# Kernel optimization log

Hardware: AMD Instinct MI355X
Metric: run time of the kernel (lower is better)

Reference implementation:

```python
import jax, jax.numpy as jnp
import numpy as np

SOFT_TAU = 0.5
MAX_TEMP = 40.0
LABEL_SMOOTH = 0.1


def setup_inputs() -> dict:
    key = jax.random.key(0)
    k1, k2 = jax.random.split(key)
    B, Tv, Tw, D = 64, 128, 128, 256
    video_features = jax.random.normal(k1, (B, Tv, D), dtype=jnp.float32)
    wifi_features = jax.random.normal(k2, (B, Tw, D), dtype=jnp.float32)
    logit_scale = jnp.ones((), dtype=jnp.float32)
    return {"video_features": video_features, "wifi_features": wifi_features, "logit_scale": logit_scale}


def _cross_entropy_ls(logits, labels):
    # torch CrossEntropyLoss(label_smoothing=0.1), mean reduction
    logp = jax.nn.log_softmax(logits, axis=-1)
    nll = -jnp.take_along_axis(logp, labels[:, None], axis=1)[:, 0]
    smooth = -jnp.mean(logp, axis=-1)
    return jnp.mean((1.0 - LABEL_SMOOTH) * nll + LABEL_SMOOTH * smooth)


def reference(video_features, wifi_features, logit_scale):
    B = video_features.shape[0]
    # [B, B, Tv, Tw] dense cross-modal similarity
    sim = jnp.einsum('imd,jnd->ijmn', video_features, wifi_features)
    sim_d = jax.lax.stop_gradient(sim)
    # video->wifi soft pooling over Tw
    attn_v2w = jax.nn.softmax(sim_d / SOFT_TAU, axis=3)
    soft_sim_v2w = jnp.sum(sim * attn_v2w, axis=3)  # [B, B, Tv]
    # wifi->video soft pooling over Tv
    attn_w2v = jax.nn.softmax(sim_d / SOFT_TAU, axis=2)
    soft_sim_w2v = jnp.sum(sim * attn_w2v, axis=2)  # [B, B, Tw]
    # frame-level softmax pooling to global similarity
    fw_v = jax.nn.softmax(jax.lax.stop_gradient(soft_sim_v2w) / SOFT_TAU, axis=2)
    sim_v2w_global = jnp.sum(soft_sim_v2w * fw_v, axis=2)  # [B, B]
    fw_w = jax.nn.softmax(jax.lax.stop_gradient(soft_sim_w2v) / SOFT_TAU, axis=2)
    sim_w2v_global = jnp.sum(soft_sim_w2v * fw_w, axis=2)  # [B, B]
    dense_similarity = (sim_v2w_global + sim_w2v_global) / 2.0
    scale = jnp.minimum(logit_scale, MAX_TEMP)
    logits_per_video = scale * dense_similarity
    logits_per_wifi = logits_per_video.T
    labels = jnp.arange(B, dtype=jnp.int32)
    loss_video = _cross_entropy_ls(logits_per_video, labels)
    loss_wifi = _cross_entropy_ls(logits_per_wifi, labels)
    return (loss_video + loss_wifi) / 2.0
```

## Files before the change

kernel.cpp:

```cpp
#include <hip/hip_runtime.h>
#include <hip/hip_bf16.h>

typedef __attribute__((ext_vector_type(8))) short bf16x8;
typedef __attribute__((ext_vector_type(16))) float f32x16;
typedef __attribute__((ext_vector_type(4))) unsigned short u16x4;

#define TT 128
#define DD 256
#define BK 64

__device__ __forceinline__ unsigned short f2bf(float f) {
  unsigned int x = __float_as_uint(f);
  x += 0x7fffu + ((x >> 16) & 1u);
  return (unsigned short)(x >> 16);
}

__device__ __forceinline__ bf16x8 pack8(float4 lo, float4 hi) {
  bf16x8 v;
  v[0] = (short)f2bf(lo.x); v[1] = (short)f2bf(lo.y);
  v[2] = (short)f2bf(lo.z); v[3] = (short)f2bf(lo.w);
  v[4] = (short)f2bf(hi.x); v[5] = (short)f2bf(hi.y);
  v[6] = (short)f2bf(hi.z); v[7] = (short)f2bf(hi.w);
  return v;
}

__global__ __launch_bounds__(256) void conv_kernel(
    const float* __restrict__ v, const float* __restrict__ w,
    unsigned short* __restrict__ vb, unsigned short* __restrict__ wb) {
  const int idx = blockIdx.x * 256 + threadIdx.x;
  float4 a = reinterpret_cast<const float4*>(v)[idx];
  float4 b = reinterpret_cast<const float4*>(w)[idx];
  u16x4 pa, pb;
  pa[0] = f2bf(a.x); pa[1] = f2bf(a.y); pa[2] = f2bf(a.z); pa[3] = f2bf(a.w);
  pb[0] = f2bf(b.x); pb[1] = f2bf(b.y); pb[2] = f2bf(b.z); pb[3] = f2bf(b.w);
  reinterpret_cast<u16x4*>(vb)[idx] = pa;
  reinterpret_cast<u16x4*>(wb)[idx] = pb;
}

template <bool PRE>
__global__ __launch_bounds__(512, 4) void pair_kernel(
    const float* __restrict__ videof, const float* __restrict__ wifif,
    const unsigned short* __restrict__ videob,
    const unsigned short* __restrict__ wifib,
    float* __restrict__ dense) {
  __shared__ __align__(16) char lds[73728];
  const int tid = threadIdx.x;
  const int bid = blockIdx.x;
  const int bi = bid >> 6, bj = bid & 63;
  const int wid = tid >> 6, l = tid & 63;
  const int l31 = l & 31;

  const int o  = wid >> 2;
  const int mg = wid & 1;
  const int cg = (wid >> 1) & 1;

  const char* vsrc = (const char*)videob + (size_t)bi * (TT * DD * 2);
  const char* wsrc = (const char*)wifib  + (size_t)bj * (TT * DD * 2);
  const int grow8 = l >> 3;
  const int gcb   = ((l & 7) ^ grow8) << 4;
  const int srow = tid >> 2;
  const int scb  = (tid & 3) * 32;
  const int sswz = (srow & 7) << 4;
  const int sb0  = srow * 128 + ((scb) ^ sswz);
  const int sb1  = srow * 128 + ((scb + 16) ^ sswz);

  f32x16 acc[2][2];
#pragma unroll
  for (int mi = 0; mi < 2; ++mi)
#pragma unroll
    for (int t = 0; t < 2; ++t)
#pragma unroll
      for (int r = 0; r < 16; ++r) acc[mi][t][r] = 0.f;

  const int apan = o ? 16384 : 0;
  const int bpan = o ? 0 : 16384;
  const int xr   = (l & 7) << 4;
  const int khalf = (l >> 5) * 16;
  const int x0 = (mg * 64 + l31) * 128;
  const int x1 = (mg * 64 + 32 + l31) * 128;
  const int y0 = (cg * 64 + l31) * 128;
  const int y1 = (cg * 64 + 32 + l31) * 128;

#define STAGE_PRE(KP, BUF)                                                    \
  do {                                                                        \
    _Pragma("unroll") for (int k_ = 0; k_ < 4; ++k_) {                        \
      const int q_ = wid * 4 + k_;                                            \
      const int c_ = q_ & 15;                                                 \
      const char* s_ = ((q_ < 16) ? vsrc : wsrc) + (c_ * 8 + grow8) * 512 +   \
                       (KP) * 128 + gcb;                                      \
      char* d_ = lds + (BUF) * 32768 + ((q_ < 16) ? 0 : 16384) + c_ * 1024;   \
      __builtin_amdgcn_global_load_lds((const void*)s_, (void*)d_, 16, 0, 0); \
    }                                                                         \
  } while (0)

#define STAGE_REG(KP, BUF)                                                    \
  do {                                                                        \
    const float* pa_ = videof + (size_t)bi * (TT * DD) + srow * DD +          \
                       (KP) * BK + (tid & 3) * 16;                            \
    const float* pb_ = wifif + (size_t)bj * (TT * DD) + srow * DD +           \
                       (KP) * BK + (tid & 3) * 16;                            \
    float4 a0_ = *(const float4*)(pa_);                                       \
    float4 a1_ = *(const float4*)(pa_ + 4);                                   \
    float4 a2_ = *(const float4*)(pa_ + 8);                                   \
    float4 a3_ = *(const float4*)(pa_ + 12);                                  \
    float4 b0_ = *(const float4*)(pb_);                                       \
    float4 b1_ = *(const float4*)(pb_ + 4);                                   \
    float4 b2_ = *(const float4*)(pb_ + 8);                                   \
    float4 b3_ = *(const float4*)(pb_ + 12);                                  \
    char* base_ = lds + (BUF) * 32768;                                        \
    *(bf16x8*)(base_ + sb0)         = pack8(a0_, a1_);                        \
    *(bf16x8*)(base_ + sb1)         = pack8(a2_, a3_);                        \
    *(bf16x8*)(base_ + 16384 + sb0) = pack8(b0_, b1_);                        \
    *(bf16x8*)(base_ + 16384 + sb1) = pack8(b2_, b3_);                        \
  } while (0)

  if constexpr (PRE) STAGE_PRE(0, 0); else STAGE_REG(0, 0);
  __syncthreads();

  for (int kp = 0; kp < 4; ++kp) {
    const int bufoff = (kp & 1) * 32768;
    if (kp < 3) {
      if constexpr (PRE) STAGE_PRE(kp + 1, (kp + 1) & 1);
      else STAGE_REG(kp + 1, (kp + 1) & 1);
    }
#pragma unroll
    for (int ks = 0; ks < 4; ++ks) {
      const int cb = ks * 32 + khalf;
      bf16x8 ax0 = *(const bf16x8*)(lds + bufoff + apan + x0 + (cb ^ xr));
      bf16x8 ax1 = *(const bf16x8*)(lds + bufoff + apan + x1 + (cb ^ xr));
      bf16x8 by0 = *(const bf16x8*)(lds + bufoff + bpan + y0 + (cb ^ xr));
      bf16x8 by1 = *(const bf16x8*)(lds + bufoff + bpan + y1 + (cb ^ xr));
      acc[0][0] = __builtin_amdgcn_mfma_f32_32x32x16_bf16(ax0, by0, acc[0][0], 0, 0, 0);
      acc[0][1] = __builtin_amdgcn_mfma_f32_32x32x16_bf16(ax0, by1, acc[0][1], 0, 0, 0);
      acc[1][0] = __builtin_amdgcn_mfma_f32_32x32x16_bf16(ax1, by0, acc[1][0], 0, 0, 0);
      acc[1][1] = __builtin_amdgcn_mfma_f32_32x32x16_bf16(ax1, by1, acc[1][1], 0, 0, 0);
    }
    __syncthreads();
  }

  float* PM = (float*)(lds + 65536);
  float* PS = PM + 512;
  float* PV = PM + 1024;
  float* Gb = PM + 1536;
  const int colb = cg * 64;

#pragma unroll
  for (int t = 0; t < 2; ++t) {
    float mx = acc[0][t][0];
#pragma unroll
    for (int mi = 0; mi < 2; ++mi)
#pragma unroll
      for (int r = 0; r < 16; ++r) mx = fmaxf(mx, acc[mi][t][r]);
    mx = fmaxf(mx, __shfl_xor(mx, 32));
    if (l < 32) PM[o * 256 + mg * 128 + colb + t * 32 + l] = mx;
  }
  __syncthreads();

#pragma unroll
  for (int t = 0; t < 2; ++t) {
    const int c = colb + t * 32 + l31;
    const float mx = fmaxf(PM[o * 256 + c], PM[o * 256 + 128 + c]);
    float se = 0.f, sv = 0.f;
#pragma unroll
    for (int mi = 0; mi < 2; ++mi)
#pragma unroll
      for (int r = 0; r < 16; ++r) {
        const float v = acc[mi][t][r];
        const float e = __expf((v - mx) * 2.0f);
        se += e;
        sv = fmaf(e, v, sv);
      }
    se += __shfl_xor(se, 32);
    sv += __shfl_xor(sv, 32);
    if (l < 32) {
      PS[o * 256 + mg * 128 + c] = se;
      PV[o * 256 + mg * 128 + c] = sv;
    }
  }
  __syncthreads();

  if (wid < 2) {
    const int oo = wid == 0 ? 1 : 0;
    const float* PSo = PS + oo * 256;
    const float* PVo = PV + oo * 256;
    float a0 = (PVo[l] + PVo[128 + l]) / (PSo[l] + PSo[128 + l]);
    float a1 = (PVo[64 + l] + PVo[192 + l]) / (PSo[64 + l] + PSo[192 + l]);
    float mx = fmaxf(a0, a1);
#pragma unroll
    for (int s = 1; s < 64; s <<= 1) mx = fmaxf(mx, __shfl_xor(mx, s));
    float e0 = __expf((a0 - mx) * 2.0f), e1 = __expf((a1 - mx) * 2.0f);
    float se = e0 + e1, sev = e0 * a0 + e1 * a1;
#pragma unroll
    for (int s = 1; s < 64; s <<= 1) { se += __shfl_xor(se, s); sev += __shfl_xor(sev, s); }
    if (l == 0) Gb[wid] = sev / se;
  }
  __syncthreads();
  if (tid == 0) dense[bid] = 0.5f * (Gb[0] + Gb[1]);
}

__global__ __launch_bounds__(64) void loss_kernel(
    const float* __restrict__ dense, const float* __restrict__ scalep,
    float* __restrict__ out) {
  const int i = threadIdx.x;
  const float sc = fminf(scalep[0], 40.0f);
  float mxr = -3.4e38f, mxc = -3.4e38f;
  for (int j = 0; j < 64; ++j) {
    mxr = fmaxf(mxr, sc * dense[i * 64 + j]);
    mxc = fmaxf(mxc, sc * dense[j * 64 + i]);
  }
  float ser = 0.f, sec = 0.f, slr = 0.f, slc = 0.f;
  for (int j = 0; j < 64; ++j) {
    float zr = sc * dense[i * 64 + j];
    float zc = sc * dense[j * 64 + i];
    ser += __expf(zr - mxr); sec += __expf(zc - mxc);
    slr += zr;               slc += zc;
  }
  const float lser = mxr + logf(ser);
  const float lsec = mxc + logf(sec);
  const float zd = sc * dense[i * 65];
  float lv = lser - 0.9f * zd - 0.1f * (slr * (1.0f / 64.0f));
  float lw = lsec - 0.9f * zd - 0.1f * (slc * (1.0f / 64.0f));
  float t = 0.5f * (lv + lw);
#pragma unroll
  for (int s = 1; s < 64; s <<= 1) t += __shfl_xor(t, s);
  if (i == 0) out[0] = t * (1.0f / 64.0f);
}

extern "C" void kernel_launch(void* const* d_in, const int* in_sizes, int n_in,
                              void* d_out, int out_size, void* d_ws, size_t ws_size,
                              hipStream_t stream) {
  (void)in_sizes; (void)n_in; (void)out_size;
  const float* video = (const float*)d_in[0];
  const float* wifi  = (const float*)d_in[1];
  const float* scale = (const float*)d_in[2];
  float* dense = (float*)d_ws;
  unsigned short* vb = (unsigned short*)((char*)d_ws + 16384);
  unsigned short* wb = vb + 64 * TT * DD;

  const bool pre = ws_size >= (size_t)16384 + 2u * 64 * TT * DD * 2;
  if (pre) {
    hipLaunchKernelGGL(conv_kernel, dim3(2048), dim3(256), 0, stream,
                       video, wifi, vb, wb);
    hipLaunchKernelGGL((pair_kernel<true>), dim3(64 * 64), dim3(512), 0, stream,
                       video, wifi, vb, wb, dense);
  } else {
    hipLaunchKernelGGL((pair_kernel<false>), dim3(64 * 64), dim3(512), 0, stream,
                       video, wifi, vb, wb, dense);
  }
  hipLaunchKernelGGL(loss_kernel, dim3(1), dim3(64), 0, stream,
                     dense, scale, (float*)d_out);
}
```

Before: 101.7 us.

## Halve pair-kernel block to 4 waves, each computing a 64x128 MFMA tile

Shrinks the pair kernel from 8 to 4 wavefronts per block. Each wave now holds a 2x4 grid of 32x32 MFMA accumulators covering all 128 columns instead of 2x2, and staging loops issue twice as many loads per thread. This raises register-level reuse of A fragments and cuts cross-wave LDS traffic. The cost is doubled accumulator registers, which lowers occupancy (launch bounds 256,2), and less parallelism for hiding load latency.

```diff
diff --git a/kernel.cpp b/kernel.cpp
--- a/kernel.cpp
+++ b/kernel.cpp
@@ -38,7 +38,7 @@
 }
 
 template <bool PRE>
-__global__ __launch_bounds__(512, 4) void pair_kernel(
+__global__ __launch_bounds__(256, 2) void pair_kernel(
     const float* __restrict__ videof, const float* __restrict__ wifif,
     const unsigned short* __restrict__ videob,
     const unsigned short* __restrict__ wifib,
@@ -50,41 +50,36 @@
   const int wid = tid >> 6, l = tid & 63;
   const int l31 = l & 31;
 
-  const int o  = wid >> 2;
+  const int o  = wid >> 1;
   const int mg = wid & 1;
-  const int cg = (wid >> 1) & 1;
 
   const char* vsrc = (const char*)videob + (size_t)bi * (TT * DD * 2);
   const char* wsrc = (const char*)wifib  + (size_t)bj * (TT * DD * 2);
   const int grow8 = l >> 3;
   const int gcb   = ((l & 7) ^ grow8) << 4;
-  const int srow = tid >> 2;
-  const int scb  = (tid & 3) * 32;
+  const int srow = tid >> 1;
+  const int scb  = (tid & 1) * 64;
   const int sswz = (srow & 7) << 4;
-  const int sb0  = srow * 128 + ((scb) ^ sswz);
-  const int sb1  = srow * 128 + ((scb + 16) ^ sswz);
-
-  f32x16 acc[2][2];
+
+  f32x16 acc[2][4];
 #pragma unroll
   for (int mi = 0; mi < 2; ++mi)
 #pragma unroll
-    for (int t = 0; t < 2; ++t)
+    for (int t = 0; t < 4; ++t)
 #pragma unroll
       for (int r = 0; r < 16; ++r) acc[mi][t][r] = 0.f;
 
   const int apan = o ? 16384 : 0;
   const int bpan = o ? 0 : 16384;
-  const int xr   = (l & 7) << 4;
+  const int xr    = (l & 7) << 4;
   const int khalf = (l >> 5) * 16;
   const int x0 = (mg * 64 + l31) * 128;
-  const int x1 = (mg * 64 + 32 + l31) * 128;
-  const int y0 = (cg * 64 + l31) * 128;
-  const int y1 = (cg * 64 + 32 + l31) * 128;
+  const int y0 = l31 * 128;
 
 #define STAGE_PRE(KP, BUF)                                                    \
   do {                                                                        \
-    _Pragma("unroll") for (int k_ = 0; k_ < 4; ++k_) {                        \
-      const int q_ = wid * 4 + k_;                                            \
+    _Pragma("unroll") for (int k_ = 0; k_ < 8; ++k_) {                        \
+      const int q_ = wid * 8 + k_;                                            \
       const int c_ = q_ & 15;                                                 \
       const char* s_ = ((q_ < 16) ? vsrc : wsrc) + (c_ * 8 + grow8) * 512 +   \
                        (KP) * 128 + gcb;                                      \
@@ -96,22 +91,26 @@
 #define STAGE_REG(KP, BUF)                                                    \
   do {                                                                        \
     const float* pa_ = videof + (size_t)bi * (TT * DD) + srow * DD +          \
-                       (KP) * BK + (tid & 3) * 16;                            \
+                       (KP) * BK + (tid & 1) * 32;                            \
     const float* pb_ = wifif + (size_t)bj * (TT * DD) + srow * DD +           \
-                       (KP) * BK + (tid & 3) * 16;                            \
-    float4 a0_ = *(const float4*)(pa_);                                       \
-    float4 a1_ = *(const float4*)(pa_ + 4);                                   \
-    float4 a2_ = *(const float4*)(pa_ + 8);                                   \
-    float4 a3_ = *(const float4*)(pa_ + 12);                                  \
-    float4 b0_ = *(const float4*)(pb_);                                       \
-    float4 b1_ = *(const float4*)(pb_ + 4);                                   \
-    float4 b2_ = *(const float4*)(pb_ + 8);                                   \
-    float4 b3_ = *(const float4*)(pb_ + 12);                                  \
+                       (KP) * BK + (tid & 1) * 32;                            \
     char* base_ = lds + (BUF) * 32768;                                        \
-    *(bf16x8*)(base_ + sb0)         = pack8(a0_, a1_);                        \
-    *(bf16x8*)(base_ + sb1)         = pack8(a2_, a3_);                        \
-    *(bf16x8*)(base_ + 16384 + sb0) = pack8(b0_, b1_);                        \
-    *(bf16x8*)(base_ + 16384 + sb1) = pack8(b2_, b3_);                        \
+    _Pragma("unroll") for (int h_ = 0; h_ < 2; ++h_) {                        \
+      float4 a0_ = *(const float4*)(pa_ + h_ * 16);                           \
+      float4 a1_ = *(const float4*)(pa_ + h_ * 16 + 4);                       \
+      float4 a2_ = *(const float4*)(pa_ + h_ * 16 + 8);                       \
+      float4 a3_ = *(const float4*)(pa_ + h_ * 16 + 12);                      \
+      float4 b0_ = *(const float4*)(pb_ + h_ * 16);                           \
+      float4 b1_ = *(const float4*)(pb_ + h_ * 16 + 4);                       \
+      float4 b2_ = *(const float4*)(pb_ + h_ * 16 + 8);                       \
+      float4 b3_ = *(const float4*)(pb_ + h_ * 16 + 12);                      \
+      const int c0_ = srow * 128 + ((scb + h_ * 32) ^ sswz);                  \
+      const int c1_ = srow * 128 + ((scb + h_ * 32 + 16) ^ sswz);             \
+      *(bf16x8*)(base_ + c0_)         = pack8(a0_, a1_);                      \
+      *(bf16x8*)(base_ + c1_)         = pack8(a2_, a3_);                      \
+      *(bf16x8*)(base_ + 16384 + c0_) = pack8(b0_, b1_);                      \
+      *(bf16x8*)(base_ + 16384 + c1_) = pack8(b2_, b3_);                      \
+    }                                                                         \
   } while (0)
 
   if constexpr (PRE) STAGE_PRE(0, 0); else STAGE_REG(0, 0);
@@ -126,14 +125,22 @@
 #pragma unroll
     for (int ks = 0; ks < 4; ++ks) {
       const int cb = ks * 32 + khalf;
-      bf16x8 ax0 = *(const bf16x8*)(lds + bufoff + apan + x0 + (cb ^ xr));
-      bf16x8 ax1 = *(const bf16x8*)(lds + bufoff + apan + x1 + (cb ^ xr));
-      bf16x8 by0 = *(const bf16x8*)(lds + bufoff + bpan + y0 + (cb ^ xr));
-      bf16x8 by1 = *(const bf16x8*)(lds + bufoff + bpan + y1 + (cb ^ xr));
+      const char* xb = lds + bufoff + apan;
+      const char* yb = lds + bufoff + bpan;
+      bf16x8 ax0 = *(const bf16x8*)(xb + x0 + (cb ^ xr));
+      bf16x8 ax1 = *(const bf16x8*)(xb + x0 + 4096 + (cb ^ xr));
+      bf16x8 by0 = *(const bf16x8*)(yb + y0 + (cb ^ xr));
+      bf16x8 by1 = *(const bf16x8*)(yb + y0 + 4096 + (cb ^ xr));
+      bf16x8 by2 = *(const bf16x8*)(yb + y0 + 8192 + (cb ^ xr));
+      bf16x8 by3 = *(const bf16x8*)(yb + y0 + 12288 + (cb ^ xr));
       acc[0][0] = __builtin_amdgcn_mfma_f32_32x32x16_bf16(ax0, by0, acc[0][0], 0, 0, 0);
       acc[0][1] = __builtin_amdgcn_mfma_f32_32x32x16_bf16(ax0, by1, acc[0][1], 0, 0, 0);
+      acc[0][2] = __builtin_amdgcn_mfma_f32_32x32x16_bf16(ax0, by2, acc[0][2], 0, 0, 0);
+      acc[0][3] = __builtin_amdgcn_mfma_f32_32x32x16_bf16(ax0, by3, acc[0][3], 0, 0, 0);
       acc[1][0] = __builtin_amdgcn_mfma_f32_32x32x16_bf16(ax1, by0, acc[1][0], 0, 0, 0);
       acc[1][1] = __builtin_amdgcn_mfma_f32_32x32x16_bf16(ax1, by1, acc[1][1], 0, 0, 0);
+      acc[1][2] = __builtin_amdgcn_mfma_f32_32x32x16_bf16(ax1, by2, acc[1][2], 0, 0, 0);
+      acc[1][3] = __builtin_amdgcn_mfma_f32_32x32x16_bf16(ax1, by3, acc[1][3], 0, 0, 0);
     }
     __syncthreads();
   }
@@ -142,23 +149,22 @@
   float* PS = PM + 512;
   float* PV = PM + 1024;
   float* Gb = PM + 1536;
-  const int colb = cg * 64;
-
-#pragma unroll
-  for (int t = 0; t < 2; ++t) {
+
+#pragma unroll
+  for (int t = 0; t < 4; ++t) {
     float mx = acc[0][t][0];
 #pragma unroll
     for (int mi = 0; mi < 2; ++mi)
 #pragma unroll
       for (int r = 0; r < 16; ++r) mx = fmaxf(mx, acc[mi][t][r]);
     mx = fmaxf(mx, __shfl_xor(mx, 32));
-    if (l < 32) PM[o * 256 + mg * 128 + colb + t * 32 + l] = mx;
-  }
-  __syncthreads();
-
-#pragma unroll
-  for (int t = 0; t < 2; ++t) {
-    const int c = colb + t * 32 + l31;
+    if (l < 32) PM[o * 256 + mg * 128 + t * 32 + l] = mx;
+  }
+  __syncthreads();
+
+#pragma unroll
+  for (int t = 0; t < 4; ++t) {
+    const int c = t * 32 + l31;
     const float mx = fmaxf(PM[o * 256 + c], PM[o * 256 + 128 + c]);
     float se = 0.f, sv = 0.f;
 #pragma unroll
@@ -241,10 +247,10 @@
   if (pre) {
     hipLaunchKernelGGL(conv_kernel, dim3(2048), dim3(256), 0, stream,
                        video, wifi, vb, wb);
-    hipLaunchKernelGGL((pair_kernel<true>), dim3(64 * 64), dim3(512), 0, stream,
+    hipLaunchKernelGGL((pair_kernel<true>), dim3(64 * 64), dim3(256), 0, stream,
                        video, wifi, vb, wb, dense);
   } else {
-    hipLaunchKernelGGL((pair_kernel<false>), dim3(64 * 64), dim3(512), 0, stream,
+    hipLaunchKernelGGL((pair_kernel<false>), dim3(64 * 64), dim3(256), 0, stream,
                        video, wifi, vb, wb, dense);
   }
   hipLaunchKernelGGL(loss_kernel, dim3(1), dim3(64), 0, stream,
```

Result: faster. 97.41 us (-4.2%).

## Pad LDS row groups and use online-softmax partial merge in epilogue

Applied to the files above, without the earlier changes.

Changes the shared-memory tile layout so each 8-row group is padded to a 1056-byte stride, which is meant to reduce bank conflicts on MFMA operand reads. It also replaces the two-pass max/exp softmax epilogue with a per-half online softmax: each half keeps its own max, and the halves are merged with rescaling, which removes one block-wide barrier round. Exponentials move to exp2f with a folded log2e·2 constant. LDS usage grows slightly and an extra merge stage is added.

```diff
diff --git a/kernel.cpp b/kernel.cpp
--- a/kernel.cpp
+++ b/kernel.cpp
@@ -8,6 +8,11 @@
 #define TT 128
 #define DD 256
 #define BK 64
+#define CP 1056
+#define PAN (16 * CP)
+#define BUFSZ (2 * PAN)
+#define PART (2 * BUFSZ)
+#define K2L 2.8853900817779268f
 
 __device__ __forceinline__ unsigned short f2bf(float f) {
   unsigned int x = __float_as_uint(f);
@@ -43,7 +48,7 @@
     const unsigned short* __restrict__ videob,
     const unsigned short* __restrict__ wifib,
     float* __restrict__ dense) {
-  __shared__ __align__(16) char lds[73728];
+  __shared__ __align__(16) char lds[73744];
   const int tid = threadIdx.x;
   const int bid = blockIdx.x;
   const int bi = bid >> 6, bj = bid & 63;
@@ -61,8 +66,7 @@
   const int srow = tid >> 2;
   const int scb  = (tid & 3) * 32;
   const int sswz = (srow & 7) << 4;
-  const int sb0  = srow * 128 + ((scb) ^ sswz);
-  const int sb1  = srow * 128 + ((scb + 16) ^ sswz);
+  const int srbase = (srow >> 3) * CP + (srow & 7) * 128;
 
   f32x16 acc[2][2];
 #pragma unroll
@@ -72,14 +76,14 @@
 #pragma unroll
       for (int r = 0; r < 16; ++r) acc[mi][t][r] = 0.f;
 
-  const int apan = o ? 16384 : 0;
-  const int bpan = o ? 0 : 16384;
-  const int xr   = (l & 7) << 4;
+  const int apan = o ? PAN : 0;
+  const int bpan = o ? 0 : PAN;
+  const int xr    = (l31 & 7) << 4;
   const int khalf = (l >> 5) * 16;
-  const int x0 = (mg * 64 + l31) * 128;
-  const int x1 = (mg * 64 + 32 + l31) * 128;
-  const int y0 = (cg * 64 + l31) * 128;
-  const int y1 = (cg * 64 + 32 + l31) * 128;
+  const int xrow  = mg * 64 + l31;
+  const int ycol  = cg * 64 + l31;
+  const int xbase = (xrow >> 3) * CP + (xrow & 7) * 128;
+  const int ybase = (ycol >> 3) * CP + (ycol & 7) * 128;
 
 #define STAGE_PRE(KP, BUF)                                                    \
   do {                                                                        \
@@ -88,7 +92,7 @@
       const int c_ = q_ & 15;                                                 \
       const char* s_ = ((q_ < 16) ? vsrc : wsrc) + (c_ * 8 + grow8) * 512 +   \
                        (KP) * 128 + gcb;                                      \
-      char* d_ = lds + (BUF) * 32768 + ((q_ < 16) ? 0 : 16384) + c_ * 1024;   \
+      char* d_ = lds + (BUF) * BUFSZ + ((q_ < 16) ? 0 : PAN) + c_ * CP;       \
       __builtin_amdgcn_global_load_lds((const void*)s_, (void*)d_, 16, 0, 0); \
     }                                                                         \
   } while (0)
@@ -107,29 +111,33 @@
     float4 b1_ = *(const float4*)(pb_ + 4);                                   \
     float4 b2_ = *(const float4*)(pb_ + 8);                                   \
     float4 b3_ = *(const float4*)(pb_ + 12);                                  \
-    char* base_ = lds + (BUF) * 32768;                                        \
-    *(bf16x8*)(base_ + sb0)         = pack8(a0_, a1_);                        \
-    *(bf16x8*)(base_ + sb1)         = pack8(a2_, a3_);                        \
-    *(bf16x8*)(base_ + 16384 + sb0) = pack8(b0_, b1_);                        \
-    *(bf16x8*)(base_ + 16384 + sb1) = pack8(b2_, b3_);                        \
+    char* base_ = lds + (BUF) * BUFSZ;                                        \
+    const int c0_ = srbase + ((scb) ^ sswz);                                  \
+    const int c1_ = srbase + ((scb + 16) ^ sswz);                             \
+    *(bf16x8*)(base_ + c0_)       = pack8(a0_, a1_);                          \
+    *(bf16x8*)(base_ + c1_)       = pack8(a2_, a3_);                          \
+    *(bf16x8*)(base_ + PAN + c0_) = pack8(b0_, b1_);                          \
+    *(bf16x8*)(base_ + PAN + c1_) = pack8(b2_, b3_);                          \
   } while (0)
 
   if constexpr (PRE) STAGE_PRE(0, 0); else STAGE_REG(0, 0);
   __syncthreads();
 
   for (int kp = 0; kp < 4; ++kp) {
-    const int bufoff = (kp & 1) * 32768;
+    const int bufoff = (kp & 1) * BUFSZ;
     if (kp < 3) {
       if constexpr (PRE) STAGE_PRE(kp + 1, (kp + 1) & 1);
       else STAGE_REG(kp + 1, (kp + 1) & 1);
     }
+    const char* xb = lds + bufoff + apan + xbase;
+    const char* yb = lds + bufoff + bpan + ybase;
 #pragma unroll
     for (int ks = 0; ks < 4; ++ks) {
-      const int cb = ks * 32 + khalf;
-      bf16x8 ax0 = *(const bf16x8*)(lds + bufoff + apan + x0 + (cb ^ xr));
-      bf16x8 ax1 = *(const bf16x8*)(lds + bufoff + apan + x1 + (cb ^ xr));
-      bf16x8 by0 = *(const bf16x8*)(lds + bufoff + bpan + y0 + (cb ^ xr));
-      bf16x8 by1 = *(const bf16x8*)(lds + bufoff + bpan + y1 + (cb ^ xr));
+      const int off = (ks * 32 + khalf) ^ xr;
+      bf16x8 ax0 = *(const bf16x8*)(xb + off);
+      bf16x8 ax1 = *(const bf16x8*)(xb + 4 * CP + off);
+      bf16x8 by0 = *(const bf16x8*)(yb + off);
+      bf16x8 by1 = *(const bf16x8*)(yb + 4 * CP + off);
       acc[0][0] = __builtin_amdgcn_mfma_f32_32x32x16_bf16(ax0, by0, acc[0][0], 0, 0, 0);
       acc[0][1] = __builtin_amdgcn_mfma_f32_32x32x16_bf16(ax0, by1, acc[0][1], 0, 0, 0);
       acc[1][0] = __builtin_amdgcn_mfma_f32_32x32x16_bf16(ax1, by0, acc[1][0], 0, 0, 0);
@@ -138,58 +146,65 @@
     __syncthreads();
   }
 
-  float* PM = (float*)(lds + 65536);
+  float* PM = (float*)(lds + PART);
   float* PS = PM + 512;
   float* PV = PM + 1024;
   float* Gb = PM + 1536;
-  const int colb = cg * 64;
 
 #pragma unroll
   for (int t = 0; t < 2; ++t) {
     float mx = acc[0][t][0];
 #pragma unroll
-    for (int mi = 0; mi < 2; ++mi)
-#pragma unroll
-      for (int r = 0; r < 16; ++r) mx = fmaxf(mx, acc[mi][t][r]);
-    mx = fmaxf(mx, __shfl_xor(mx, 32));
-    if (l < 32) PM[o * 256 + mg * 128 + colb + t * 32 + l] = mx;
-  }
-  __syncthreads();
-
-#pragma unroll
-  for (int t = 0; t < 2; ++t) {
-    const int c = colb + t * 32 + l31;
-    const float mx = fmaxf(PM[o * 256 + c], PM[o * 256 + 128 + c]);
+    for (int r = 1; r < 16; ++r) mx = fmaxf(mx, acc[0][t][r]);
+#pragma unroll
+    for (int r = 0; r < 16; ++r) mx = fmaxf(mx, acc[1][t][r]);
+    const float mxk = mx * K2L;
     float se = 0.f, sv = 0.f;
 #pragma unroll
     for (int mi = 0; mi < 2; ++mi)
 #pragma unroll
       for (int r = 0; r < 16; ++r) {
         const float v = acc[mi][t][r];
-        const float e = __expf((v - mx) * 2.0f);
+        const float e = exp2f(fmaf(v, K2L, -mxk));
         se += e;
         sv = fmaf(e, v, sv);
       }
-    se += __shfl_xor(se, 32);
-    sv += __shfl_xor(sv, 32);
+    const float om = __shfl_xor(mx, 32);
+    const float os = __shfl_xor(se, 32);
+    const float ov = __shfl_xor(sv, 32);
+    const float M  = fmaxf(mx, om);
+    const float f1 = exp2f((mx - M) * K2L);
+    const float f2 = exp2f((om - M) * K2L);
+    se = fmaf(se, f1, os * f2);
+    sv = fmaf(sv, f1, ov * f2);
     if (l < 32) {
-      PS[o * 256 + mg * 128 + c] = se;
-      PV[o * 256 + mg * 128 + c] = sv;
+      const int idx = o * 256 + mg * 128 + cg * 64 + t * 32 + l;
+      PM[idx] = M; PS[idx] = se; PV[idx] = sv;
     }
   }
   __syncthreads();
 
+  if (tid < 256) {
+    const int o2 = tid >> 7, c = tid & 127;
+    const int i0 = o2 * 256 + c, i1 = i0 + 128;
+    const float m0 = PM[i0], m1 = PM[i1];
+    const float M  = fmaxf(m0, m1);
+    const float f0 = exp2f((m0 - M) * K2L);
+    const float f1 = exp2f((m1 - M) * K2L);
+    const float s  = fmaf(PS[i0], f0, PS[i1] * f1);
+    const float v  = fmaf(PV[i0], f0, PV[i1] * f1);
+    PM[i0] = v / s;
+  }
+  __syncthreads();
+
   if (wid < 2) {
-    const int oo = wid == 0 ? 1 : 0;
-    const float* PSo = PS + oo * 256;
-    const float* PVo = PV + oo * 256;
-    float a0 = (PVo[l] + PVo[128 + l]) / (PSo[l] + PSo[128 + l]);
-    float a1 = (PVo[64 + l] + PVo[192 + l]) / (PSo[64 + l] + PSo[192 + l]);
+    const float* RS = PM + (wid == 0 ? 256 : 0);
+    float a0 = RS[l], a1 = RS[64 + l];
     float mx = fmaxf(a0, a1);
 #pragma unroll
     for (int s = 1; s < 64; s <<= 1) mx = fmaxf(mx, __shfl_xor(mx, s));
-    float e0 = __expf((a0 - mx) * 2.0f), e1 = __expf((a1 - mx) * 2.0f);
-    float se = e0 + e1, sev = e0 * a0 + e1 * a1;
+    float e0 = exp2f((a0 - mx) * K2L), e1 = exp2f((a1 - mx) * K2L);
+    float se = e0 + e1, sev = fmaf(e0, a0, e1 * a1);
 #pragma unroll
     for (int s = 1; s < 64; s <<= 1) { se += __shfl_xor(se, s); sev += __shfl_xor(sev, s); }
     if (l == 0) Gb[wid] = sev / se;
```

Result: slower. 111.2 us (+9.4%).

## Keep video fragments in registers and loop over sixteen wifi clips per block

Applied to the files above, without the earlier changes.

The pair kernel becomes persistent-style: 256 blocks, each loading one video clip's bf16 fragments into registers once and streaming 16 wifi clips through double-buffered LDS halves. The per-pair epilogue now does an online max/sum merge with exp2 instead of an extra LDS max pass and barrier. The final reduction overlaps the next clip's loads and writes results via atomicAdd into zero-initialised outputs. This trades grid parallelism (256 blocks, launch bound lowered to 2 waves/EU) and heavier register use for less redundant video loading and fewer barriers.

```diff
diff --git a/kernel.cpp b/kernel.cpp
--- a/kernel.cpp
+++ b/kernel.cpp
@@ -7,7 +7,9 @@
 
 #define TT 128
 #define DD 256
-#define BK 64
+#define HBUF 32768
+#define PARTOFF 65536
+#define K2L 2.8853900817779268f
 
 __device__ __forceinline__ unsigned short f2bf(float f) {
   unsigned int x = __float_as_uint(f);
@@ -37,165 +39,196 @@
   reinterpret_cast<u16x4*>(wb)[idx] = pb;
 }
 
+#define FR(BUF, ROW, KSLOT)                                                   \
+  (*(const bf16x8*)(lds + (BUF) * HBUF + (ROW) * 256 +                        \
+                    ((((KSLOT)) ^ ((ROW) & 15)) << 4)))
+
 template <bool PRE>
-__global__ __launch_bounds__(512, 4) void pair_kernel(
+__global__ __launch_bounds__(512, 2) void pair_kernel(
     const float* __restrict__ videof, const float* __restrict__ wifif,
     const unsigned short* __restrict__ videob,
     const unsigned short* __restrict__ wifib,
     float* __restrict__ dense) {
-  __shared__ __align__(16) char lds[73728];
+  __shared__ __align__(16) char lds[77824];
   const int tid = threadIdx.x;
   const int bid = blockIdx.x;
-  const int bi = bid >> 6, bj = bid & 63;
+  const int i  = bid >> 2, jg = bid & 3;
   const int wid = tid >> 6, l = tid & 63;
   const int l31 = l & 31;
+  const int khalf = l >> 5;
 
   const int o  = wid >> 2;
   const int mg = wid & 1;
   const int cg = (wid >> 1) & 1;
 
-  const char* vsrc = (const char*)videob + (size_t)bi * (TT * DD * 2);
-  const char* wsrc = (const char*)wifib  + (size_t)bj * (TT * DD * 2);
-  const int grow8 = l >> 3;
-  const int gcb   = ((l & 7) ^ grow8) << 4;
-  const int srow = tid >> 2;
-  const int scb  = (tid & 3) * 32;
-  const int sswz = (srow & 7) << 4;
-  const int sb0  = srow * 128 + ((scb) ^ sswz);
-  const int sb1  = srow * 128 + ((scb + 16) ^ sswz);
+  if (tid < 16) dense[i * 64 + jg * 16 + tid] = 0.0f;
+
+  const char* vsrc  = (const char*)videob + (size_t)i * (TT * DD * 2);
+  const char* wsrc0 = (const char*)wifib + (size_t)(jg * 16) * (TT * DD * 2);
+  const float* vsrcf  = videof + (size_t)i * (TT * DD);
+  const float* wsrcf0 = wifif + (size_t)(jg * 16) * (TT * DD);
+
+  const int crow  = l >> 4;
+  const int cslot = l & 15;
+  const int frow = tid >> 2, fq = tid & 3;
+
+  const int vbase = (o ? cg : mg) * 64;
+  const int wbase = (o ? mg : cg) * 64;
+
+#define STAGE_PRE_(SRC, KH, BUF)                                              \
+  do {                                                                        \
+    _Pragma("unroll") for (int k_ = 0; k_ < 4; ++k_) {                        \
+      const int c_ = wid * 4 + k_;                                            \
+      const int r_ = c_ * 4 + crow;                                           \
+      const char* s_ = (SRC) + r_ * 512 + (KH) * 256 +                        \
+                       ((cslot ^ (r_ & 15)) << 4);                            \
+      char* d_ = lds + (BUF) * HBUF + c_ * 1024;                              \
+      __builtin_amdgcn_global_load_lds((const void*)s_, (void*)d_, 16, 0, 0); \
+    }                                                                         \
+  } while (0)
+
+#define STAGE_REG_(SRCF, KH, BUF)                                             \
+  do {                                                                        \
+    _Pragma("unroll") for (int s_ = 0; s_ < 4; ++s_) {                        \
+      const int slot_ = fq * 4 + s_;                                          \
+      const float* p_ = (SRCF) + frow * DD + (KH) * 128 + slot_ * 8;          \
+      float4 x0_ = *(const float4*)(p_);                                      \
+      float4 x1_ = *(const float4*)(p_ + 4);                                  \
+      *(bf16x8*)(lds + (BUF) * HBUF + frow * 256 +                            \
+                 ((slot_ ^ (frow & 15)) << 4)) = pack8(x0_, x1_);             \
+    }                                                                         \
+  } while (0)
+
+  if constexpr (PRE) STAGE_PRE_(vsrc, 0, 0); else STAGE_REG_(vsrcf, 0, 0);
+  __syncthreads();
+  if constexpr (PRE) STAGE_PRE_(vsrc, 1, 1); else STAGE_REG_(vsrcf, 1, 1);
+  bf16x8 vf[2][16];
+#pragma unroll
+  for (int g = 0; g < 2; ++g)
+#pragma unroll
+    for (int ksl = 0; ksl < 8; ++ksl)
+      vf[g][ksl] = FR(0, vbase + g * 32 + l31, 2 * ksl + khalf);
+  __syncthreads();
+  if constexpr (PRE) STAGE_PRE_(wsrc0, 0, 0); else STAGE_REG_(wsrcf0, 0, 0);
+#pragma unroll
+  for (int g = 0; g < 2; ++g)
+#pragma unroll
+    for (int ksl = 0; ksl < 8; ++ksl)
+      vf[g][8 + ksl] = FR(1, vbase + g * 32 + l31, 2 * ksl + khalf);
+  __syncthreads();
 
   f32x16 acc[2][2];
-#pragma unroll
-  for (int mi = 0; mi < 2; ++mi)
-#pragma unroll
-    for (int t = 0; t < 2; ++t)
-#pragma unroll
-      for (int r = 0; r < 16; ++r) acc[mi][t][r] = 0.f;
-
-  const int apan = o ? 16384 : 0;
-  const int bpan = o ? 0 : 16384;
-  const int xr   = (l & 7) << 4;
-  const int khalf = (l >> 5) * 16;
-  const int x0 = (mg * 64 + l31) * 128;
-  const int x1 = (mg * 64 + 32 + l31) * 128;
-  const int y0 = (cg * 64 + l31) * 128;
-  const int y1 = (cg * 64 + 32 + l31) * 128;
-
-#define STAGE_PRE(KP, BUF)                                                    \
-  do {                                                                        \
-    _Pragma("unroll") for (int k_ = 0; k_ < 4; ++k_) {                        \
-      const int q_ = wid * 4 + k_;                                            \
-      const int c_ = q_ & 15;                                                 \
-      const char* s_ = ((q_ < 16) ? vsrc : wsrc) + (c_ * 8 + grow8) * 512 +   \
-                       (KP) * 128 + gcb;                                      \
-      char* d_ = lds + (BUF) * 32768 + ((q_ < 16) ? 0 : 16384) + c_ * 1024;   \
-      __builtin_amdgcn_global_load_lds((const void*)s_, (void*)d_, 16, 0, 0); \
-    }                                                                         \
-  } while (0)
-
-#define STAGE_REG(KP, BUF)                                                    \
-  do {                                                                        \
-    const float* pa_ = videof + (size_t)bi * (TT * DD) + srow * DD +          \
-                       (KP) * BK + (tid & 3) * 16;                            \
-    const float* pb_ = wifif + (size_t)bj * (TT * DD) + srow * DD +           \
-                       (KP) * BK + (tid & 3) * 16;                            \
-    float4 a0_ = *(const float4*)(pa_);                                       \
-    float4 a1_ = *(const float4*)(pa_ + 4);                                   \
-    float4 a2_ = *(const float4*)(pa_ + 8);                                   \
-    float4 a3_ = *(const float4*)(pa_ + 12);                                  \
-    float4 b0_ = *(const float4*)(pb_);                                       \
-    float4 b1_ = *(const float4*)(pb_ + 4);                                   \
-    float4 b2_ = *(const float4*)(pb_ + 8);                                   \
-    float4 b3_ = *(const float4*)(pb_ + 12);                                  \
-    char* base_ = lds + (BUF) * 32768;                                        \
-    *(bf16x8*)(base_ + sb0)         = pack8(a0_, a1_);                        \
-    *(bf16x8*)(base_ + sb1)         = pack8(a2_, a3_);                        \
-    *(bf16x8*)(base_ + 16384 + sb0) = pack8(b0_, b1_);                        \
-    *(bf16x8*)(base_ + 16384 + sb1) = pack8(b2_, b3_);                        \
-  } while (0)
-
-  if constexpr (PRE) STAGE_PRE(0, 0); else STAGE_REG(0, 0);
-  __syncthreads();
-
-  for (int kp = 0; kp < 4; ++kp) {
-    const int bufoff = (kp & 1) * 32768;
-    if (kp < 3) {
-      if constexpr (PRE) STAGE_PRE(kp + 1, (kp + 1) & 1);
-      else STAGE_REG(kp + 1, (kp + 1) & 1);
+
+#define COMPUTE(BUF, KOFF)                                                    \
+  do {                                                                        \
+    _Pragma("unroll") for (int ksl = 0; ksl < 8; ++ksl) {                     \
+      const int kslot_ = 2 * ksl + khalf;                                     \
+      bf16x8 w0_ = FR(BUF, wbase + l31, kslot_);                              \
+      bf16x8 w1_ = FR(BUF, wbase + 32 + l31, kslot_);                         \
+      bf16x8 v0_ = vf[0][(KOFF) + ksl];                                       \
+      bf16x8 v1_ = vf[1][(KOFF) + ksl];                                       \
+      if (o == 0) {                                                           \
+        acc[0][0] = __builtin_amdgcn_mfma_f32_32x32x16_bf16(v0_, w0_, acc[0][0], 0, 0, 0); \
+        acc[0][1] = __builtin_amdgcn_mfma_f32_32x32x16_bf16(v0_, w1_, acc[0][1], 0, 0, 0); \
+        acc[1][0] = __builtin_amdgcn_mfma_f32_32x32x16_bf16(v1_, w0_, acc[1][0], 0, 0, 0); \
+        acc[1][1] = __builtin_amdgcn_mfma_f32_32x32x16_bf16(v1_, w1_, acc[1][1], 0, 0, 0); \
+      } else {                                                                \
+        acc[0][0] = __builtin_amdgcn_mfma_f32_32x32x16_bf16(w0_, v0_, acc[0][0], 0, 0, 0); \
+        acc[0][1] = __builtin_amdgcn_mfma_f32_32x32x16_bf16(w0_, v1_, acc[0][1], 0, 0, 0); \
+        acc[1][0] = __builtin_amdgcn_mfma_f32_32x32x16_bf16(w1_, v0_, acc[1][0], 0, 0, 0); \
+        acc[1][1] = __builtin_amdgcn_mfma_f32_32x32x16_bf16(w1_, v1_, acc[1][1], 0, 0, 0); \
+      }                                                                       \
+    }                                                                         \
+  } while (0)
+
+#define EPILOGUE(JJ)                                                          \
+  do {                                                                        \
+    float* P_ = (float*)(lds + PARTOFF + ((JJ) & 1) * 6144);                  \
+    _Pragma("unroll") for (int t = 0; t < 2; ++t) {                           \
+      float mx = acc[0][t][0];                                                \
+      _Pragma("unroll") for (int r = 1; r < 16; ++r) mx = fmaxf(mx, acc[0][t][r]); \
+      _Pragma("unroll") for (int r = 0; r < 16; ++r) mx = fmaxf(mx, acc[1][t][r]); \
+      const float mxk = mx * K2L;                                             \
+      float se = 0.f, sv = 0.f;                                               \
+      _Pragma("unroll") for (int mi = 0; mi < 2; ++mi)                        \
+        _Pragma("unroll") for (int r = 0; r < 16; ++r) {                      \
+          const float v = acc[mi][t][r];                                      \
+          const float e = exp2f(fmaf(v, K2L, -mxk));                          \
+          se += e; sv = fmaf(e, v, sv);                                       \
+        }                                                                     \
+      const float om = __shfl_xor(mx, 32);                                    \
+      const float os = __shfl_xor(se, 32);                                    \
+      const float ov = __shfl_xor(sv, 32);                                    \
+      const float M = fmaxf(mx, om);                                          \
+      const float f1 = exp2f((mx - M) * K2L);                                 \
+      const float f2 = exp2f((om - M) * K2L);                                 \
+      se = fmaf(se, f1, os * f2);                                             \
+      sv = fmaf(sv, f1, ov * f2);                                             \
+      if (l < 32) {                                                           \
+        const int idx_ = o * 256 + mg * 128 + cg * 64 + t * 32 + l;           \
+        P_[idx_] = M; P_[512 + idx_] = se; P_[1024 + idx_] = sv;              \
+      }                                                                       \
+    }                                                                         \
+  } while (0)
+
+#define REDUCE(JJ)                                                            \
+  do {                                                                        \
+    const float* P_ = (const float*)(lds + PARTOFF + ((JJ) & 1) * 6144);      \
+    const int oo_ = (wid == 0) ? 1 : 0;                                       \
+    float a0_, a1_;                                                           \
+    {                                                                         \
+      const int c_ = oo_ * 256 + l;                                           \
+      const float m0 = P_[c_], m1 = P_[c_ + 128];                             \
+      const float M = fmaxf(m0, m1);                                          \
+      const float f0 = exp2f((m0 - M) * K2L);                                 \
+      const float f1 = exp2f((m1 - M) * K2L);                                 \
+      a0_ = fmaf(P_[1024 + c_], f0, P_[1024 + c_ + 128] * f1) /               \
+            fmaf(P_[512 + c_], f0, P_[512 + c_ + 128] * f1);                  \
+    }                                                                         \
+    {                                                                         \
+      const int c_ = oo_ * 256 + 64 + l;                                      \
+      const float m0 = P_[c_], m1 = P_[c_ + 128];                             \
+      const float M = fmaxf(m0, m1);                                          \
+      const float f0 = exp2f((m0 - M) * K2L);                                 \
+      const float f1 = exp2f((m1 - M) * K2L);                                 \
+      a1_ = fmaf(P_[1024 + c_], f0, P_[1024 + c_ + 128] * f1) /               \
+            fmaf(P_[512 + c_], f0, P_[512 + c_ + 128] * f1);                  \
+    }                                                                         \
+    float mx_ = fmaxf(a0_, a1_);                                              \
+    _Pragma("unroll") for (int s_ = 1; s_ < 64; s_ <<= 1)                     \
+      mx_ = fmaxf(mx_, __shfl_xor(mx_, s_));                                  \
+    const float e0_ = exp2f((a0_ - mx_) * K2L);                               \
+    const float e1_ = exp2f((a1_ - mx_) * K2L);                               \
+    float se_ = e0_ + e1_, sev_ = fmaf(e0_, a0_, e1_ * a1_);                  \
+    _Pragma("unroll") for (int s_ = 1; s_ < 64; s_ <<= 1) {                   \
+      se_ += __shfl_xor(se_, s_); sev_ += __shfl_xor(sev_, s_);               \
+    }                                                                         \
+    if (l == 0)                                                               \
+      atomicAdd(dense + i * 64 + jg * 16 + (JJ), 0.5f * (sev_ / se_));        \
+  } while (0)
+
+  for (int jj = 0; jj < 16; ++jj) {
+    const char* wsJ1  = wsrc0 + (size_t)jj * (TT * DD * 2);
+    const float* wsJ1f = wsrcf0 + (size_t)jj * (TT * DD);
+    if constexpr (PRE) STAGE_PRE_(wsJ1, 1, 1); else STAGE_REG_(wsJ1f, 1, 1);
+#pragma unroll
+    for (int mi = 0; mi < 2; ++mi)
+#pragma unroll
+      for (int t = 0; t < 2; ++t)
+#pragma unroll
+        for (int r = 0; r < 16; ++r) acc[mi][t][r] = 0.f;
+    COMPUTE(0, 0);
+    __syncthreads();
+    if (jj < 15) {
+      const char* wsJ2  = wsrc0 + (size_t)(jj + 1) * (TT * DD * 2);
+      const float* wsJ2f = wsrcf0 + (size_t)(jj + 1) * (TT * DD);
+      if constexpr (PRE) STAGE_PRE_(wsJ2, 0, 0); else STAGE_REG_(wsJ2f, 0, 0);
     }
-#pragma unroll
-    for (int ks = 0; ks < 4; ++ks) {
-      const int cb = ks * 32 + khalf;
-      bf16x8 ax0 = *(const bf16x8*)(lds + bufoff + apan + x0 + (cb ^ xr));
-      bf16x8 ax1 = *(const bf16x8*)(lds + bufoff + apan + x1 + (cb ^ xr));
-      bf16x8 by0 = *(const bf16x8*)(lds + bufoff + bpan + y0 + (cb ^ xr));
-      bf16x8 by1 = *(const bf16x8*)(lds + bufoff + bpan + y1 + (cb ^ xr));
-      acc[0][0] = __builtin_amdgcn_mfma_f32_32x32x16_bf16(ax0, by0, acc[0][0], 0, 0, 0);
-      acc[0][1] = __builtin_amdgcn_mfma_f32_32x32x16_bf16(ax0, by1, acc[0][1], 0, 0, 0);
-      acc[1][0] = __builtin_amdgcn_mfma_f32_32x32x16_bf16(ax1, by0, acc[1][0], 0, 0, 0);
-      acc[1][1] = __builtin_amdgcn_mfma_f32_32x32x16_bf16(ax1, by1, acc[1][1], 0, 0, 0);
-    }
+    COMPUTE(1, 8);
+    EPILOGUE(jj);
     __syncthreads();
-  }
-
-  float* PM = (float*)(lds + 65536);
-  float* PS = PM + 512;
-  float* PV = PM + 1024;
-  float* Gb = PM + 1536;
-  const int colb = cg * 64;
-
-#pragma unroll
-  for (int t = 0; t < 2; ++t) {
-    float mx = acc[0][t][0];
-#pragma unroll
-    for (int mi = 0; mi < 2; ++mi)
-#pragma unroll
-      for (int r = 0; r < 16; ++r) mx = fmaxf(mx, acc[mi][t][r]);
-    mx = fmaxf(mx, __shfl_xor(mx, 32));
-    if (l < 32) PM[o * 256 + mg * 128 + colb + t * 32 + l] = mx;
-  }
-  __syncthreads();
-
-#pragma unroll
-  for (int t = 0; t < 2; ++t) {
-    const int c = colb + t * 32 + l31;
-    const float mx = fmaxf(PM[o * 256 + c], PM[o * 256 + 128 + c]);
-    float se = 0.f, sv = 0.f;
-#pragma unroll
-    for (int mi = 0; mi < 2; ++mi)
-#pragma unroll
-      for (int r = 0; r < 16; ++r) {
-        const float v = acc[mi][t][r];
-        const float e = __expf((v - mx) * 2.0f);
-        se += e;
-        sv = fmaf(e, v, sv);
-      }
-    se += __shfl_xor(se, 32);
-    sv += __shfl_xor(sv, 32);
-    if (l < 32) {
-      PS[o * 256 + mg * 128 + c] = se;
-      PV[o * 256 + mg * 128 + c] = sv;
-    }
-  }
-  __syncthreads();
-
-  if (wid < 2) {
-    const int oo = wid == 0 ? 1 : 0;
-    const float* PSo = PS + oo * 256;
-    const float* PVo = PV + oo * 256;
-    float a0 = (PVo[l] + PVo[128 + l]) / (PSo[l] + PSo[128 + l]);
-    float a1 = (PVo[64 + l] + PVo[192 + l]) / (PSo[64 + l] + PSo[192 + l]);
-    float mx = fmaxf(a0, a1);
-#pragma unroll
-    for (int s = 1; s < 64; s <<= 1) mx = fmaxf(mx, __shfl_xor(mx, s));
-    float e0 = __expf((a0 - mx) * 2.0f), e1 = __expf((a1 - mx) * 2.0f);
-    float se = e0 + e1, sev = e0 * a0 + e1 * a1;
-#pragma unroll
-    for (int s = 1; s < 64; s <<= 1) { se += __shfl_xor(se, s); sev += __shfl_xor(sev, s); }
-    if (l == 0) Gb[wid] = sev / se;
-  }
-  __syncthreads();
-  if (tid == 0) dense[bid] = 0.5f * (Gb[0] + Gb[1]);
+    if (wid < 2) REDUCE(jj);
+  }
 }
 
 __global__ __launch_bounds__(64) void loss_kernel(
@@ -241,10 +274,10 @@
   if (pre) {
     hipLaunchKernelGGL(conv_kernel, dim3(2048), dim3(256), 0, stream,
                        video, wifi, vb, wb);
-    hipLaunchKernelGGL((pair_kernel<true>), dim3(64 * 64), dim3(512), 0, stream,
+    hipLaunchKernelGGL((pair_kernel<true>), dim3(256), dim3(512), 0, stream,
                        video, wifi, vb, wb, dense);
   } else {
-    hipLaunchKernelGGL((pair_kernel<false>), dim3(64 * 64), dim3(512), 0, stream,
+    hipLaunchKernelGGL((pair_kernel<false>), dim3(256), dim3(512), 0, stream,
                        video, wifi, vb, wb, dense);
   }
   hipLaunchKernelGGL(loss_kernel, dim3(1), dim3(64), 0, stream,
```

Measured after the change: 108.6 us. 6.8% more time.
